# Kernel optimization log

Measured on AMD Instinct MI355X. Metric: run time of the kernel, lower is better.

The kernel has to match this reference:

```python
import jax, jax.numpy as jnp
import numpy as np
import math

B, H, N = 16, 768, 2048  # batch, hidden_size, num_patches


def setup_inputs() -> dict:
    key = jax.random.key(0)
    k1, k2, k3, k4 = jax.random.split(key, 4)
    shape = (B, H, N)
    return {
        "query": jax.random.normal(k1, shape, dtype=jnp.float32),
        "key": jax.random.normal(k2, shape, dtype=jnp.float32),
        "value": jax.random.normal(k3, shape, dtype=jnp.float32),
        "key_pe": jax.random.normal(k4, shape, dtype=jnp.float32),
    }


def reference(query, key, value, key_pe):
    # query/key/value/key_pe: [B, H, N]
    hidden_size = query.shape[1]
    scale = 1.0 / math.sqrt(hidden_size)
    # content + positional scores: [B, N, N]  (q^T k + q^T pe)
    attn = jnp.einsum('bhn,bhm->bnm', query, key) \
         + jnp.einsum('bhn,bhm->bnm', query, key_pe)
    attn = jax.nn.softmax(attn * scale, axis=-1)
    # combine with values: [B, N, N] x [B, N, H] -> [B, N, H] -> [B, H, N]
    out = jnp.einsum('bnm,bhm->bhn', attn, value)
    return out
```

## Files before the change

### kernel.cpp

```cpp
#include <hip/hip_runtime.h>

#define B_ 16
#define H_ 768
#define N_ 2048
#define SCALE 0.03608439182435161f

typedef unsigned short u16;
typedef unsigned int u32;
typedef __attribute__((ext_vector_type(8))) short short8;
typedef __attribute__((ext_vector_type(4))) float float4v;

__device__ __forceinline__ u16 f2bf(float f) {
  u32 u = __float_as_uint(f);
  u32 r = (u + 0x7FFFu + ((u >> 16) & 1u)) >> 16;
  return (u16)r;
}
__device__ __forceinline__ float bf2f(u16 h) { return __uint_as_float(((u32)h) << 16); }
__device__ __forceinline__ u32 pk2(float a, float b) {
  return (u32)f2bf(a) | ((u32)f2bf(b) << 16);
}

__device__ __forceinline__ void dma16(const void* g, void* l) {
  __builtin_amdgcn_global_load_lds(
      (const __attribute__((address_space(1))) void*)g,
      (__attribute__((address_space(3))) void*)l, 16, 0, 0);
}

__global__ __launch_bounds__(256) void kt_transpose(
    const float* __restrict__ q, const float* __restrict__ k,
    const float* __restrict__ pe, u16* __restrict__ qT, u16* __restrict__ keffT) {
  __shared__ float tile[64][65];
  const int t = threadIdx.x;
  const int b = blockIdx.z & 15;
  const int which = blockIdx.z >> 4;
  const float* src = which ? k : q;
  u16* dst = which ? keffT : qT;
  const size_t inb = (size_t)b * H_ * N_;
  const size_t outb = (size_t)b * N_ * H_;
  const int n0 = blockIdx.x * 64;
  const int h0 = blockIdx.y * 64;
  const int col = t & 63;
  const int r0 = t >> 6;
#pragma unroll
  for (int i = 0; i < 16; ++i) {
    const int row = r0 + i * 4;
    const size_t idx = inb + (size_t)(h0 + row) * N_ + (n0 + col);
    float v = src[idx];
    if (which) v += pe[idx];
    tile[row][col] = v;
  }
  __syncthreads();
  const int w = t & 31;
  const int r1 = t >> 5;
#pragma unroll
  for (int i = 0; i < 8; ++i) {
    const int row = r1 + i * 8;
    const u32 u = pk2(tile[2 * w][row], tile[2 * w + 1][row]);
    *(u32*)(dst + outb + (size_t)(n0 + row) * H_ + (h0 + 2 * w)) = u;
  }
}

__global__ __launch_bounds__(256) void kv_convert(
    const float* __restrict__ v, u16* __restrict__ vB) {
  const size_t i = ((size_t)blockIdx.x * 256 + threadIdx.x) * 8;
  float4 a = *(const float4*)&v[i];
  float4 b = *(const float4*)&v[i + 4];
  uint4 o;
  o.x = pk2(a.x, a.y);
  o.y = pk2(a.z, a.w);
  o.z = pk2(b.x, b.y);
  o.w = pk2(b.z, b.w);
  *(uint4*)&vB[i] = o;
}

__global__ __launch_bounds__(256) void k1_qk_gemm(
    const u16* __restrict__ qT, const u16* __restrict__ keffT, u16* __restrict__ S) {
  __shared__ __align__(16) u16 ldsA[128 * 32];
  __shared__ __align__(16) u16 ldsB[128 * 32];
  __shared__ __align__(16) float ldsC[32 * 132];
  const int t = threadIdx.x;
  const int lane = t & 63;
  const int wv = t >> 6;
  const int wr = wv >> 1, wc = wv & 1;
  const int b = blockIdx.z;
  const int m0 = blockIdx.x * 128;
  const int n0 = blockIdx.y * 128;
  const u16* Ab = qT + (size_t)b * N_ * H_ + (size_t)n0 * H_;
  const u16* Bb = keffT + (size_t)b * N_ * H_ + (size_t)m0 * H_;
  float4v acc[4][4] = {};
  const int fr = lane & 15;
  const int fk = (lane >> 4) * 8;
  for (int k0 = 0; k0 < H_; k0 += 32) {
    __syncthreads();
#pragma unroll
    for (int r = 0; r < 2; ++r) {
      const int c = r * 256 + t;
      const int row = c >> 2;
      const int co = (c & 3) * 8;
      dma16(Ab + (size_t)row * H_ + (k0 + co), &ldsA[c * 8]);
      dma16(Bb + (size_t)row * H_ + (k0 + co), &ldsB[c * 8]);
    }
    __syncthreads();
    short8 af[4], bfv[4];
#pragma unroll
    for (int i = 0; i < 4; ++i)
      af[i] = *(const short8*)&ldsA[(wr * 64 + i * 16 + fr) * 32 + fk];
#pragma unroll
    for (int j = 0; j < 4; ++j)
      bfv[j] = *(const short8*)&ldsB[(wc * 64 + j * 16 + fr) * 32 + fk];
#pragma unroll
    for (int i = 0; i < 4; ++i)
#pragma unroll
      for (int j = 0; j < 4; ++j)
        acc[i][j] = __builtin_amdgcn_mfma_f32_16x16x32_bf16(af[i], bfv[j], acc[i][j], 0, 0, 0);
  }
  const int cr = lane >> 4;
  const int cc = lane & 15;
  const size_t Sb = (size_t)b * N_ * N_;
  const int orow = t >> 3;
  const int ocol = (t & 7) * 16;
  for (int chunk = 0; chunk < 4; ++chunk) {
    __syncthreads();
    if (wr == (chunk >> 1)) {
#pragma unroll
      for (int ii = 0; ii < 2; ++ii) {
        const int i = (chunk & 1) * 2 + ii;
#pragma unroll
        for (int j = 0; j < 4; ++j)
#pragma unroll
          for (int r = 0; r < 4; ++r)
            ldsC[(ii * 16 + cr * 4 + r) * 132 + (wc * 64 + j * 16 + cc)] = acc[i][j][r];
      }
    }
    __syncthreads();
    const float* srcp = &ldsC[orow * 132 + ocol];
    float4 fA = *(const float4*)&srcp[0];
    float4 fB = *(const float4*)&srcp[4];
    float4 fC = *(const float4*)&srcp[8];
    float4 fD = *(const float4*)&srcp[12];
    uint4 o0, o1;
    o0.x = pk2(fA.x, fA.y); o0.y = pk2(fA.z, fA.w);
    o0.z = pk2(fB.x, fB.y); o0.w = pk2(fB.z, fB.w);
    o1.x = pk2(fC.x, fC.y); o1.y = pk2(fC.z, fC.w);
    o1.z = pk2(fD.x, fD.y); o1.w = pk2(fD.z, fD.w);
    u16* dst = S + Sb + (size_t)(n0 + chunk * 32 + orow) * N_ + (m0 + ocol);
    *(uint4*)dst = o0;
    *(uint4*)(dst + 8) = o1;
  }
}

__global__ __launch_bounds__(256) void k1b_softmax(u16* __restrict__ S) {
  const int t = threadIdx.x;
  const int lane = t & 63;
  const int wv = t >> 6;
  const size_t row = (size_t)blockIdx.x * 4 + wv;
  u16* base = S + row * N_;
  float x[32];
#pragma unroll
  for (int c = 0; c < 4; ++c) {
    uint4 u = *(const uint4*)&base[c * 512 + lane * 8];
    const u32 uu[4] = {u.x, u.y, u.z, u.w};
#pragma unroll
    for (int e = 0; e < 4; ++e) {
      x[c * 8 + e * 2] = bf2f((u16)(uu[e] & 0xFFFFu));
      x[c * 8 + e * 2 + 1] = bf2f((u16)(uu[e] >> 16));
    }
  }
  float mx = -1e30f;
#pragma unroll
  for (int e = 0; e < 32; ++e) mx = fmaxf(mx, x[e]);
#pragma unroll
  for (int off = 32; off > 0; off >>= 1) mx = fmaxf(mx, __shfl_xor(mx, off));
  float sum = 0.f;
#pragma unroll
  for (int e = 0; e < 32; ++e) {
    x[e] = __expf((x[e] - mx) * SCALE);
    sum += x[e];
  }
#pragma unroll
  for (int off = 32; off > 0; off >>= 1) sum += __shfl_xor(sum, off);
  const float rinv = 1.0f / sum;
#pragma unroll
  for (int c = 0; c < 4; ++c) {
    uint4 o;
    o.x = pk2(x[c * 8 + 0] * rinv, x[c * 8 + 1] * rinv);
    o.y = pk2(x[c * 8 + 2] * rinv, x[c * 8 + 3] * rinv);
    o.z = pk2(x[c * 8 + 4] * rinv, x[c * 8 + 5] * rinv);
    o.w = pk2(x[c * 8 + 6] * rinv, x[c * 8 + 7] * rinv);
    *(uint4*)&base[c * 512 + lane * 8] = o;
  }
}

__global__ __launch_bounds__(256) void k2_pv_gemm(
    const u16* __restrict__ vB, const u16* __restrict__ P, float* __restrict__ out) {
  __shared__ __align__(16) u16 ldsA[128 * 32];
  __shared__ __align__(16) u16 ldsB[128 * 32];
  const int t = threadIdx.x;
  const int lane = t & 63;
  const int wv = t >> 6;
  const int wr = wv >> 1, wc = wv & 1;
  const int b = blockIdx.z;
  const int n0 = blockIdx.x * 128;
  const int h0 = blockIdx.y * 128;
  const u16* Ab = vB + (size_t)b * H_ * N_ + (size_t)h0 * N_;
  const u16* Bb = P + (size_t)b * N_ * N_ + (size_t)n0 * N_;
  float4v acc[4][4] = {};
  const int fr = lane & 15;
  const int fk = (lane >> 4) * 8;
  for (int k0 = 0; k0 < N_; k0 += 32) {
    __syncthreads();
#pragma unroll
    for (int r = 0; r < 2; ++r) {
      const int c = r * 256 + t;
      const int row = c >> 2;
      const int co = (c & 3) * 8;
      dma16(Ab + (size_t)row * N_ + (k0 + co), &ldsA[c * 8]);
      dma16(Bb + (size_t)row * N_ + (k0 + co), &ldsB[c * 8]);
    }
    __syncthreads();
    short8 af[4], bfv[4];
#pragma unroll
    for (int i = 0; i < 4; ++i)
      af[i] = *(const short8*)&ldsA[(wr * 64 + i * 16 + fr) * 32 + fk];
#pragma unroll
    for (int j = 0; j < 4; ++j)
      bfv[j] = *(const short8*)&ldsB[(wc * 64 + j * 16 + fr) * 32 + fk];
#pragma unroll
    for (int i = 0; i < 4; ++i)
#pragma unroll
      for (int j = 0; j < 4; ++j)
        acc[i][j] = __builtin_amdgcn_mfma_f32_16x16x32_bf16(af[i], bfv[j], acc[i][j], 0, 0, 0);
  }
  const int cr = lane >> 4, cc = lane & 15;
  const size_t ob = (size_t)b * H_ * N_;
#pragma unroll
  for (int i = 0; i < 4; ++i) {
    const int hh = h0 + wr * 64 + i * 16 + cr * 4;
#pragma unroll
    for (int j = 0; j < 4; ++j) {
      const int nn = n0 + wc * 64 + j * 16 + cc;
#pragma unroll
      for (int r = 0; r < 4; ++r)
        out[ob + (size_t)(hh + r) * N_ + nn] = acc[i][j][r];
    }
  }
}

extern "C" void kernel_launch(void* const* d_in, const int* in_sizes, int n_in,
                              void* d_out, int out_size, void* d_ws, size_t ws_size,
                              hipStream_t stream) {
  const float* q = (const float*)d_in[0];
  const float* k = (const float*)d_in[1];
  const float* v = (const float*)d_in[2];
  const float* pe = (const float*)d_in[3];
  float* out = (float*)d_out;
  char* ws = (char*)d_ws;
  u16* qT = (u16*)ws;
  u16* keffT = (u16*)(ws + 50331648);
  u16* S = (u16*)(ws + 100663296);
  u16* vB = (u16*)ws;

  hipLaunchKernelGGL(kt_transpose, dim3(32, 12, 32), dim3(256), 0, stream, q, k, pe, qT, keffT);
  hipLaunchKernelGGL(k1_qk_gemm, dim3(16, 16, 16), dim3(256), 0, stream, qT, keffT, S);
  hipLaunchKernelGGL(kv_convert, dim3(12288), dim3(256), 0, stream, v, vB);
  hipLaunchKernelGGL(k1b_softmax, dim3(8192), dim3(256), 0, stream, S);
  hipLaunchKernelGGL(k2_pv_gemm, dim3(16, 6, 16), dim3(256), 0, stream, vB, S, out);
}
```

Before: 767.6 us.

## Enlarge QK GEMM tiles to 256x256 with double-buffered LDS and vectorize transpose

The QK^T GEMM moves from 128x128 tiles with 4 waves to 256x256 tiles with 8 waves and a 64-wide K step. LDS staging is double-buffered so the DMA of the next K slice overlaps the MFMAs on the current one. This raises arithmetic intensity per LDS load and cuts barrier count, at the cost of heavy register pressure from a 32-fragment accumulator per wave. The transpose kernel also switches to float4 loads and 8-byte stores.

```diff
diff --git a/kernel.cpp b/kernel.cpp
--- a/kernel.cpp
+++ b/kernel.cpp
@@ -39,24 +39,32 @@
   const size_t outb = (size_t)b * N_ * H_;
   const int n0 = blockIdx.x * 64;
   const int h0 = blockIdx.y * 64;
-  const int col = t & 63;
-  const int r0 = t >> 6;
-#pragma unroll
-  for (int i = 0; i < 16; ++i) {
-    const int row = r0 + i * 4;
-    const size_t idx = inb + (size_t)(h0 + row) * N_ + (n0 + col);
-    float v = src[idx];
-    if (which) v += pe[idx];
-    tile[row][col] = v;
+  const int col4 = (t & 15) * 4;
+  const int r0 = t >> 4;
+#pragma unroll
+  for (int i = 0; i < 4; ++i) {
+    const int row = r0 + i * 16;
+    const size_t idx = inb + (size_t)(h0 + row) * N_ + (n0 + col4);
+    float4 v = *(const float4*)&src[idx];
+    if (which) {
+      float4 p = *(const float4*)&pe[idx];
+      v.x += p.x; v.y += p.y; v.z += p.z; v.w += p.w;
+    }
+    tile[row][col4 + 0] = v.x;
+    tile[row][col4 + 1] = v.y;
+    tile[row][col4 + 2] = v.z;
+    tile[row][col4 + 3] = v.w;
   }
   __syncthreads();
-  const int w = t & 31;
-  const int r1 = t >> 5;
-#pragma unroll
-  for (int i = 0; i < 8; ++i) {
-    const int row = r1 + i * 8;
-    const u32 u = pk2(tile[2 * w][row], tile[2 * w + 1][row]);
-    *(u32*)(dst + outb + (size_t)(n0 + row) * H_ + (h0 + 2 * w)) = u;
+  const int w2 = t & 15;
+  const int r1 = t >> 4;
+#pragma unroll
+  for (int i = 0; i < 4; ++i) {
+    const int row = r1 + i * 16;
+    uint2 u;
+    u.x = pk2(tile[4 * w2 + 0][row], tile[4 * w2 + 1][row]);
+    u.y = pk2(tile[4 * w2 + 2][row], tile[4 * w2 + 3][row]);
+    *(uint2*)(dst + outb + (size_t)(n0 + row) * H_ + (h0 + 4 * w2)) = u;
   }
 }
 
@@ -73,79 +81,95 @@
   *(uint4*)&vB[i] = o;
 }
 
-__global__ __launch_bounds__(256) void k1_qk_gemm(
+__global__ __launch_bounds__(512, 2) void k1_qk_gemm(
     const u16* __restrict__ qT, const u16* __restrict__ keffT, u16* __restrict__ S) {
-  __shared__ __align__(16) u16 ldsA[128 * 32];
-  __shared__ __align__(16) u16 ldsB[128 * 32];
-  __shared__ __align__(16) float ldsC[32 * 132];
+  __shared__ __align__(16) u16 lds[2][2][256 * 64];
   const int t = threadIdx.x;
   const int lane = t & 63;
   const int wv = t >> 6;
-  const int wr = wv >> 1, wc = wv & 1;
+  const int wm = wv >> 2;
+  const int wn = wv & 3;
   const int b = blockIdx.z;
-  const int m0 = blockIdx.x * 128;
-  const int n0 = blockIdx.y * 128;
+  const int m0 = blockIdx.x * 256;
+  const int n0 = blockIdx.y * 256;
   const u16* Ab = qT + (size_t)b * N_ * H_ + (size_t)n0 * H_;
   const u16* Bb = keffT + (size_t)b * N_ * H_ + (size_t)m0 * H_;
-  float4v acc[4][4] = {};
+  float4v acc[8][4] = {};
   const int fr = lane & 15;
   const int fk = (lane >> 4) * 8;
-  for (int k0 = 0; k0 < H_; k0 += 32) {
-    __syncthreads();
-#pragma unroll
-    for (int r = 0; r < 2; ++r) {
-      const int c = r * 256 + t;
-      const int row = c >> 2;
-      const int co = (c & 3) * 8;
-      dma16(Ab + (size_t)row * H_ + (k0 + co), &ldsA[c * 8]);
-      dma16(Bb + (size_t)row * H_ + (k0 + co), &ldsB[c * 8]);
-    }
-    __syncthreads();
-    short8 af[4], bfv[4];
-#pragma unroll
-    for (int i = 0; i < 4; ++i)
-      af[i] = *(const short8*)&ldsA[(wr * 64 + i * 16 + fr) * 32 + fk];
-#pragma unroll
-    for (int j = 0; j < 4; ++j)
-      bfv[j] = *(const short8*)&ldsB[(wc * 64 + j * 16 + fr) * 32 + fk];
-#pragma unroll
-    for (int i = 0; i < 4; ++i)
+
+#define STAGE_K1(buf, kt)                                                     \
+  {                                                                           \
+    const int kbase = (kt)*64;                                                \
+    _Pragma("unroll") for (int r = 0; r < 4; ++r) {                           \
+      const int c = r * 512 + t;                                              \
+      const int row = c >> 3;                                                 \
+      const int k8 = (c & 7) * 8;                                             \
+      dma16(Ab + (size_t)row * H_ + (kbase + k8), &lds[buf][0][c * 8]);       \
+      dma16(Bb + (size_t)row * H_ + (kbase + k8), &lds[buf][1][c * 8]);       \
+    }                                                                         \
+  }
+
+  STAGE_K1(0, 0);
+  __syncthreads();
+  const int NT = H_ / 64;
+  for (int kt = 0; kt < NT; ++kt) {
+    const int buf = kt & 1;
+    if (kt + 1 < NT) STAGE_K1(buf ^ 1, kt + 1);
+    const u16* LA = &lds[buf][0][0];
+    const u16* LB = &lds[buf][1][0];
+#pragma unroll
+    for (int ks = 0; ks < 2; ++ks) {
+      short8 af[8], bfv[4];
+#pragma unroll
+      for (int i = 0; i < 8; ++i)
+        af[i] = *(const short8*)&LA[(wm * 128 + i * 16 + fr) * 64 + ks * 32 + fk];
 #pragma unroll
       for (int j = 0; j < 4; ++j)
-        acc[i][j] = __builtin_amdgcn_mfma_f32_16x16x32_bf16(af[i], bfv[j], acc[i][j], 0, 0, 0);
-  }
-  const int cr = lane >> 4;
-  const int cc = lane & 15;
+        bfv[j] = *(const short8*)&LB[(wn * 64 + j * 16 + fr) * 64 + ks * 32 + fk];
+#pragma unroll
+      for (int i = 0; i < 8; ++i)
+#pragma unroll
+        for (int j = 0; j < 4; ++j)
+          acc[i][j] = __builtin_amdgcn_mfma_f32_16x16x32_bf16(af[i], bfv[j], acc[i][j], 0, 0, 0);
+    }
+    __syncthreads();
+  }
+#undef STAGE_K1
+
+  float* ldsC = (float*)&lds[0][0][0];
+  const int cr = lane >> 4, cc = lane & 15;
   const size_t Sb = (size_t)b * N_ * N_;
   const int orow = t >> 3;
-  const int ocol = (t & 7) * 16;
-  for (int chunk = 0; chunk < 4; ++chunk) {
-    __syncthreads();
-    if (wr == (chunk >> 1)) {
-#pragma unroll
-      for (int ii = 0; ii < 2; ++ii) {
-        const int i = (chunk & 1) * 2 + ii;
+  const int ocol = (t & 7) * 32;
+  for (int ch = 0; ch < 4; ++ch) {
+    if (wm == (ch >> 1)) {
+#pragma unroll
+      for (int ii = 0; ii < 4; ++ii) {
+        const int i = (ch & 1) * 4 + ii;
 #pragma unroll
         for (int j = 0; j < 4; ++j)
 #pragma unroll
           for (int r = 0; r < 4; ++r)
-            ldsC[(ii * 16 + cr * 4 + r) * 132 + (wc * 64 + j * 16 + cc)] = acc[i][j][r];
+            ldsC[(ii * 16 + cr * 4 + r) * 264 + (wn * 64 + j * 16 + cc)] = acc[i][j][r];
       }
     }
     __syncthreads();
-    const float* srcp = &ldsC[orow * 132 + ocol];
-    float4 fA = *(const float4*)&srcp[0];
-    float4 fB = *(const float4*)&srcp[4];
-    float4 fC = *(const float4*)&srcp[8];
-    float4 fD = *(const float4*)&srcp[12];
-    uint4 o0, o1;
-    o0.x = pk2(fA.x, fA.y); o0.y = pk2(fA.z, fA.w);
-    o0.z = pk2(fB.x, fB.y); o0.w = pk2(fB.z, fB.w);
-    o1.x = pk2(fC.x, fC.y); o1.y = pk2(fC.z, fC.w);
-    o1.z = pk2(fD.x, fD.y); o1.w = pk2(fD.z, fD.w);
-    u16* dst = S + Sb + (size_t)(n0 + chunk * 32 + orow) * N_ + (m0 + ocol);
-    *(uint4*)dst = o0;
-    *(uint4*)(dst + 8) = o1;
+    const float* srcp = &ldsC[orow * 264 + ocol];
+    uint4 o4[4];
+#pragma unroll
+    for (int e = 0; e < 4; ++e) {
+      float4 f0 = *(const float4*)&srcp[e * 8];
+      float4 f1 = *(const float4*)&srcp[e * 8 + 4];
+      o4[e].x = pk2(f0.x, f0.y);
+      o4[e].y = pk2(f0.z, f0.w);
+      o4[e].z = pk2(f1.x, f1.y);
+      o4[e].w = pk2(f1.z, f1.w);
+    }
+    u16* dst = S + Sb + (size_t)(n0 + ch * 64 + orow) * N_ + (m0 + ocol);
+#pragma unroll
+    for (int e = 0; e < 4; ++e) *(uint4*)(dst + e * 8) = o4[e];
+    __syncthreads();
   }
 }
 
@@ -261,7 +285,7 @@
   u16* vB = (u16*)ws;
 
   hipLaunchKernelGGL(kt_transpose, dim3(32, 12, 32), dim3(256), 0, stream, q, k, pe, qT, keffT);
-  hipLaunchKernelGGL(k1_qk_gemm, dim3(16, 16, 16), dim3(256), 0, stream, qT, keffT, S);
+  hipLaunchKernelGGL(k1_qk_gemm, dim3(8, 8, 16), dim3(512), 0, stream, qT, keffT, S);
   hipLaunchKernelGGL(kv_convert, dim3(12288), dim3(256), 0, stream, v, vB);
   hipLaunchKernelGGL(k1b_softmax, dim3(8192), dim3(256), 0, stream, S);
   hipLaunchKernelGGL(k2_pv_gemm, dim3(16, 6, 16), dim3(256), 0, stream, vB, S, out);
```

Measured after the change: 728.0 us. -5.2%, faster.
